# Kernel tuning notes

Hardware: AMD Instinct MI355X
Metric: run time of the kernel (lower is better)

Reference implementation:

```python
import jax, jax.numpy as jnp
import numpy as np
from jax import lax

B, L, D = 1, 2048, 768
D_IN, N, DT_RANK, K = 1536, 16, 48, 4
EPS = 1e-5


def setup_inputs() -> dict:
    key = jax.random.key(0)
    ks = jax.random.split(key, 10)
    s = 0.02
    x = jax.random.normal(ks[0], (B, L, D), dtype=jnp.float32)
    norm_w = jnp.ones((D,), dtype=jnp.float32)
    W_in = jax.random.normal(ks[1], (D, 2 * D_IN), dtype=jnp.float32) * s
    conv_w = jax.random.normal(ks[2], (K, 1, D_IN), dtype=jnp.float32) * s  # (W, I/groups, O)
    conv_b = jnp.zeros((D_IN,), dtype=jnp.float32)
    W_x = jax.random.normal(ks[3], (D_IN, DT_RANK + 2 * N), dtype=jnp.float32) * s
    W_dt = jax.random.normal(ks[4], (DT_RANK, D_IN), dtype=jnp.float32) * s
    b_dt = jnp.zeros((D_IN,), dtype=jnp.float32)
    A_log = jnp.broadcast_to(jnp.log(jnp.arange(1, N + 1, dtype=jnp.float32)), (D_IN, N))
    Dp = jnp.ones((D_IN,), dtype=jnp.float32)
    W_out = jax.random.normal(ks[5], (D_IN, D), dtype=jnp.float32) * s
    return {"x": x, "norm_w": norm_w, "W_in": W_in, "conv_w": conv_w, "conv_b": conv_b,
            "W_x": W_x, "W_dt": W_dt, "b_dt": b_dt, "A_log": A_log, "Dp": Dp, "W_out": W_out}


def _rmsnorm(x, w):
    return x * jax.lax.rsqrt(jnp.mean(x * x, axis=-1, keepdims=True) + EPS) * w


def _selective_scan(deltaA, deltaB_u, C):
    # deltaA, deltaB_u: (b, l, d_in, n); C: (b, l, n)
    def combine(s1, s2):
        f1, x1 = s1
        f2, x2 = s2
        return (f2 * f1, f2 * x1 + x2)
    _, xs = lax.associative_scan(combine, (deltaA, deltaB_u), axis=1)
    return jnp.einsum('bldn,bln->bld', xs, C)


def _mamba_block(x, W_in, conv_w, conv_b, W_x, W_dt, b_dt, A_log, Dp, W_out):
    b, l, d = x.shape
    xr = x @ W_in                                 # (b, l, 2*d_in)
    xs, res = jnp.split(xr, [D_IN], axis=-1)
    # depthwise causal-ish conv, padding = K-1 both sides, then trim to l
    xs = lax.conv_general_dilated(
        xs, conv_w, window_strides=(1,), padding=[(K - 1, K - 1)],
        dimension_numbers=('NWC', 'WIO', 'NWC'), feature_group_count=D_IN)
    xs = (xs + conv_b)[:, :l, :]
    u = jax.nn.silu(xs)
    # SSM
    A = -jnp.exp(A_log)                           # (d_in, n)
    x_dbl = u @ W_x                               # (b, l, dt_rank + 2n)
    delta, Bm, Cm = jnp.split(x_dbl, [DT_RANK, DT_RANK + N], axis=-1)
    delta = jax.nn.softplus(delta @ W_dt + b_dt)  # (b, l, d_in)
    deltaA = jnp.exp(jnp.einsum('bld,dn->bldn', delta, A))
    deltaB_u = jnp.einsum('bld,bln,bld->bldn', delta, Bm, u)
    y = _selective_scan(deltaA, deltaB_u, Cm) + u * Dp
    y = y * jax.nn.silu(res)
    return y @ W_out


def reference(x, norm_w, W_in, conv_w, conv_b, W_x, W_dt, b_dt, A_log, Dp, W_out):
    return _mamba_block(_rmsnorm(x, norm_w), W_in, conv_w, conv_b,
                        W_x, W_dt, b_dt, A_log, Dp, W_out) + x
```

## Files before the change

kernel.cpp:

```cpp
#include <hip/hip_runtime.h>
#include <hip/hip_bf16.h>

typedef unsigned short u16;
typedef __bf16 bfx8 __attribute__((ext_vector_type(8)));
typedef float fx4 __attribute__((ext_vector_type(4)));
typedef unsigned short ushort8 __attribute__((ext_vector_type(8)));

#define DEV __device__ __forceinline__

static constexpr int Lq = 2048, Dq = 768, DIN = 1536, NST = 16;
static constexpr int NCH = 128, LC = 16;

DEV u16 f2bf(float x) {
    union { float f; unsigned u; } v; v.f = x;
    unsigned r = v.u + 0x7fff + ((v.u >> 16) & 1);
    return (u16)(r >> 16);
}
DEV float bf2f(u16 v) {
    union { unsigned u; float f; } w; w.u = ((unsigned)v) << 16; return w.f;
}
DEV void gll16(const u16* g, u16* l) {
    __builtin_amdgcn_global_load_lds(
        (const __attribute__((address_space(1))) unsigned int*)g,
        (__attribute__((address_space(3))) unsigned int*)l, 16, 0, 0);
}

struct TD { const float* src; u16* dst; int R, C, Rp, Cp, nbx, blk0; };

__global__ __launch_bounds__(256) void prep(TD t0, TD t1, TD t2, TD t3,
                                            const float* __restrict__ x,
                                            const float* __restrict__ nw,
                                            u16* __restrict__ xn) {
    __shared__ float tile[32][33];
    __shared__ float wsum[4];
    int b = blockIdx.x;
    if (b < 3744) {
        TD td = t0;
        if (b >= t3.blk0) td = t3; else if (b >= t2.blk0) td = t2; else if (b >= t1.blk0) td = t1;
        int local = b - td.blk0;
        int c0 = (local % td.nbx) * 32, r0 = (local / td.nbx) * 32;
        int tx = threadIdx.x & 31, ty = threadIdx.x >> 5;
        #pragma unroll
        for (int i = ty; i < 32; i += 8) {
            int r = r0 + i, c = c0 + tx;
            tile[i][tx] = (r < td.R && c < td.C) ? td.src[(size_t)r * td.C + c] : 0.f;
        }
        __syncthreads();
        #pragma unroll
        for (int i = ty; i < 32; i += 8) {
            int c = c0 + i, r = r0 + tx;
            if (c < td.Cp && r < td.Rp) td.dst[(size_t)c * td.Rp + r] = f2bf(tile[tx][i]);
        }
    } else {
        int t = b - 3744;
        const float* row = x + (size_t)t * Dq;
        float ss = 0.f;
        for (int i = threadIdx.x; i < Dq; i += 256) { float a = row[i]; ss += a * a; }
        #pragma unroll
        for (int o = 32; o > 0; o >>= 1) ss += __shfl_xor(ss, o, 64);
        if ((threadIdx.x & 63) == 0) wsum[threadIdx.x >> 6] = ss;
        __syncthreads();
        ss = wsum[0] + wsum[1] + wsum[2] + wsum[3];
        float scale = rsqrtf(ss * (1.f / Dq) + 1e-5f);
        for (int i = threadIdx.x; i < Dq; i += 256)
            xn[(size_t)t * Dq + i] = f2bf(row[i] * scale * nw[i]);
    }
}

template<int BM, int BN, int EPI>
__global__ __launch_bounds__(256) void gemm_nt(const u16* __restrict__ A, const u16* __restrict__ BT,
                                               float* __restrict__ C, u16* __restrict__ Cb,
                                               const float* __restrict__ R,
                                               const float* __restrict__ bias,
                                               int M, int N, int K) {
    constexpr int BK = 64;
    constexpr int WM = BM / 2, WN = BN / 2, MI = WM / 16, NI = WN / 16;
    __shared__ u16 As[BM * BK];
    __shared__ u16 Bs[BN * BK];
    const int tid = threadIdx.x, lane = tid & 63, wid = tid >> 6;
    const int wr = wid >> 1, wc = wid & 1;
    const int bm0 = blockIdx.y * BM, bn0 = blockIdx.x * BN;
    const int li = lane & 15, g = lane >> 4;

    fx4 acc[MI][NI];
    #pragma unroll
    for (int mi = 0; mi < MI; mi++)
        #pragma unroll
        for (int ni = 0; ni < NI; ni++)
            #pragma unroll
            for (int q = 0; q < 4; q++) acc[mi][ni][q] = 0.f;

    for (int kt = 0; kt < K; kt += BK) {
        #pragma unroll
        for (int i = 0; i < (BM * 8) / 256; i++) {
            int cb = i * 256 + wid * 64;
            int c = cb + lane;
            int row = c >> 3, c16 = (c & 7) ^ (row & 7);
            gll16(A + (size_t)(bm0 + row) * K + kt + c16 * 8, &As[cb * 8]);
        }
        #pragma unroll
        for (int i = 0; i < (BN * 8) / 256; i++) {
            int cb = i * 256 + wid * 64;
            int c = cb + lane;
            int row = c >> 3, c16 = (c & 7) ^ (row & 7);
            gll16(BT + (size_t)(bn0 + row) * K + kt + c16 * 8, &Bs[cb * 8]);
        }
        __syncthreads();
        bfx8 af[MI][2], bfr[NI][2];
        #pragma unroll
        for (int mi = 0; mi < MI; mi++) {
            int row = wr * WM + mi * 16 + li;
            #pragma unroll
            for (int ks = 0; ks < 2; ks++)
                af[mi][ks] = *(const bfx8*)&As[row * BK + (((ks * 4 + g) ^ (row & 7)) * 8)];
        }
        #pragma unroll
        for (int ni = 0; ni < NI; ni++) {
            int row = wc * WN + ni * 16 + li;
            #pragma unroll
            for (int ks = 0; ks < 2; ks++)
                bfr[ni][ks] = *(const bfx8*)&Bs[row * BK + (((ks * 4 + g) ^ (row & 7)) * 8)];
        }
        #pragma unroll
        for (int ks = 0; ks < 2; ks++)
            #pragma unroll
            for (int mi = 0; mi < MI; mi++)
                #pragma unroll
                for (int ni = 0; ni < NI; ni++)
                    acc[mi][ni] = __builtin_amdgcn_mfma_f32_16x16x32_bf16(
                        af[mi][ks], bfr[ni][ks], acc[mi][ni], 0, 0, 0);
        __syncthreads();
    }

    #pragma unroll
    for (int mi = 0; mi < MI; mi++)
        #pragma unroll
        for (int ni = 0; ni < NI; ni++)
            #pragma unroll
            for (int q = 0; q < 4; q++) {
                int row = bm0 + wr * WM + mi * 16 + g * 4 + q;
                int col = bn0 + wc * WN + ni * 16 + li;
                size_t idx = (size_t)row * N + col;
                float v = acc[mi][ni][q];
                if constexpr (EPI == 0) {
                    if (R) v += R[idx];
                    C[idx] = v;
                } else if constexpr (EPI == 3) {
                    Cb[idx] = f2bf(v);
                } else if constexpr (EPI == 4) {
                    v += bias[col];
                    Cb[idx] = f2bf((v > 20.f) ? v : log1pf(__expf(v)));
                } else if constexpr (EPI == 5) {
                    C[idx] = v;
                    if (col < 64) Cb[(size_t)row * 64 + col] = f2bf(v);
                }
            }
}

__global__ __launch_bounds__(256) void conv_silu(const u16* __restrict__ xrb,
                                                 const float* __restrict__ cw,
                                                 const float* __restrict__ cb,
                                                 u16* __restrict__ ubf) {
    int i = blockIdx.x * 256 + threadIdx.x;
    int t = i / (DIN / 8), d8 = (i - t * (DIN / 8)) * 8;
    float acc[8];
    #pragma unroll
    for (int j = 0; j < 8; j++) acc[j] = cb[d8 + j];
    #pragma unroll
    for (int k = 0; k < 4; k++) {
        int tt = t - 3 + k;
        if (tt < 0) continue;
        ushort8 xv = *(const ushort8*)(xrb + (size_t)tt * (2 * DIN) + d8);
        #pragma unroll
        for (int j = 0; j < 8; j++) acc[j] = fmaf(bf2f(xv[j]), cw[k * DIN + d8 + j], acc[j]);
    }
    ushort8 o;
    #pragma unroll
    for (int j = 0; j < 8; j++) {
        float s = acc[j] / (1.f + __expf(-acc[j]));
        o[j] = f2bf(s);
    }
    *(ushort8*)(ubf + (size_t)i * 8) = o;
}

__global__ __launch_bounds__(256) void scan_p1(const u16* __restrict__ deltab, const u16* __restrict__ ubf,
                                               const float* __restrict__ xdbl, const float* __restrict__ A_log,
                                               float* __restrict__ chA, float* __restrict__ chX) {
    const int c = blockIdx.x;
    const int d = blockIdx.y * 256 + threadIdx.x;
    float An[NST];
    #pragma unroll
    for (int i = 0; i < 4; i++) {
        float4 a = *(const float4*)(A_log + (size_t)d * NST + i * 4);
        An[i * 4 + 0] = -__expf(a.x); An[i * 4 + 1] = -__expf(a.y);
        An[i * 4 + 2] = -__expf(a.z); An[i * 4 + 3] = -__expf(a.w);
    }
    float s[NST];
    #pragma unroll
    for (int n = 0; n < NST; n++) s[n] = 0.f;
    float sdl = 0.f;
    const int t0 = c * LC;
    #pragma unroll
    for (int tt = 0; tt < LC; tt++) {
        int t = t0 + tt;
        float dl = bf2f(deltab[(size_t)t * DIN + d]);
        float uu = bf2f(ubf[(size_t)t * DIN + d]);
        float dlu = dl * uu;
        #pragma unroll
        for (int i = 0; i < 4; i++) {
            float4 b = *(const float4*)(xdbl + (size_t)t * 128 + 48 + i * 4);
            float dA0 = __expf(dl * An[i*4+0]); s[i*4+0] = fmaf(dA0, s[i*4+0], dlu * b.x);
            float dA1 = __expf(dl * An[i*4+1]); s[i*4+1] = fmaf(dA1, s[i*4+1], dlu * b.y);
            float dA2 = __expf(dl * An[i*4+2]); s[i*4+2] = fmaf(dA2, s[i*4+2], dlu * b.z);
            float dA3 = __expf(dl * An[i*4+3]); s[i*4+3] = fmaf(dA3, s[i*4+3], dlu * b.w);
        }
        sdl += dl;
    }
    #pragma unroll
    for (int n = 0; n < NST; n++) {
        size_t idx = (size_t)n * (NCH * DIN) + (size_t)c * DIN + d;
        chX[idx] = s[n];
        chA[idx] = __expf(An[n] * sdl);
    }
}

__global__ __launch_bounds__(256) void scan_p2(float* __restrict__ chA, const float* __restrict__ chX) {
    int fid = blockIdx.x;
    int n = fid / 6, dd = (fid % 6) * 256 + threadIdx.x;
    size_t base = (size_t)n * (NCH * DIN) + dd;
    float s2 = 0.f;
    for (int cc = 0; cc < NCH; cc++) {
        size_t idx = base + (size_t)cc * DIN;
        float a = chA[idx], xv = chX[idx];
        chA[idx] = s2;
        s2 = fmaf(a, s2, xv);
    }
}

__global__ __launch_bounds__(256) void scan_p3(const u16* __restrict__ deltab, const u16* __restrict__ ubf,
                                               const float* __restrict__ xdbl, const float* __restrict__ A_log,
                                               const float* __restrict__ init, const float* __restrict__ Dp,
                                               const u16* __restrict__ xrb, u16* __restrict__ ybf) {
    const int c = blockIdx.x;
    const int d = blockIdx.y * 256 + threadIdx.x;
    float An[NST];
    #pragma unroll
    for (int i = 0; i < 4; i++) {
        float4 a = *(const float4*)(A_log + (size_t)d * NST + i * 4);
        An[i * 4 + 0] = -__expf(a.x); An[i * 4 + 1] = -__expf(a.y);
        An[i * 4 + 2] = -__expf(a.z); An[i * 4 + 3] = -__expf(a.w);
    }
    float s[NST];
    #pragma unroll
    for (int n = 0; n < NST; n++)
        s[n] = init[(size_t)n * (NCH * DIN) + (size_t)c * DIN + d];
    float Dpd = Dp[d];
    const int t0 = c * LC;
    #pragma unroll
    for (int tt = 0; tt < LC; tt++) {
        int t = t0 + tt;
        float dl = bf2f(deltab[(size_t)t * DIN + d]);
        float uu = bf2f(ubf[(size_t)t * DIN + d]);
        float dlu = dl * uu;
        float p = 0.f;
        #pragma unroll
        for (int i = 0; i < 4; i++) {
            float4 b  = *(const float4*)(xdbl + (size_t)t * 128 + 48 + i * 4);
            float4 cc = *(const float4*)(xdbl + (size_t)t * 128 + 64 + i * 4);
            float dA0 = __expf(dl * An[i*4+0]); s[i*4+0] = fmaf(dA0, s[i*4+0], dlu * b.x); p = fmaf(s[i*4+0], cc.x, p);
            float dA1 = __expf(dl * An[i*4+1]); s[i*4+1] = fmaf(dA1, s[i*4+1], dlu * b.y); p = fmaf(s[i*4+1], cc.y, p);
            float dA2 = __expf(dl * An[i*4+2]); s[i*4+2] = fmaf(dA2, s[i*4+2], dlu * b.z); p = fmaf(s[i*4+2], cc.z, p);
            float dA3 = __expf(dl * An[i*4+3]); s[i*4+3] = fmaf(dA3, s[i*4+3], dlu * b.w); p = fmaf(s[i*4+3], cc.w, p);
        }
        float res = bf2f(xrb[(size_t)t * (2 * DIN) + DIN + d]);
        float y = fmaf(uu, Dpd, p) * (res / (1.f + __expf(-res)));
        ybf[(size_t)t * DIN + d] = f2bf(y);
    }
}

extern "C" void kernel_launch(void* const* d_in, const int* in_sizes, int n_in,
                              void* d_out, int out_size, void* d_ws, size_t ws_size,
                              hipStream_t stream) {
    const float* x      = (const float*)d_in[0];
    const float* norm_w = (const float*)d_in[1];
    const float* W_in   = (const float*)d_in[2];
    const float* conv_w = (const float*)d_in[3];
    const float* conv_b = (const float*)d_in[4];
    const float* W_x    = (const float*)d_in[5];
    const float* W_dt   = (const float*)d_in[6];
    const float* b_dt   = (const float*)d_in[7];
    const float* A_log  = (const float*)d_in[8];
    const float* Dp     = (const float*)d_in[9];
    const float* W_out  = (const float*)d_in[10];
    float* out = (float*)d_out;

    char* wp = (char*)d_ws;
    auto alloc = [&](size_t bytes) { char* p = wp; wp += (bytes + 255) & ~(size_t)255; return p; };
    u16*      WinT   = (u16*)alloc((size_t)3072 * 768 * 2);
    u16*      WoutT  = (u16*)alloc((size_t)768 * 1536 * 2);
    u16*      WxT    = (u16*)alloc((size_t)128 * 1536 * 2);
    u16*      WdtT   = (u16*)alloc((size_t)1536 * 64 * 2);
    u16*      xn     = (u16*)alloc((size_t)Lq * Dq * 2);
    u16*      xrb    = (u16*)alloc((size_t)Lq * 3072 * 2);
    u16*      ubf    = (u16*)alloc((size_t)Lq * DIN * 2);
    float*    xdbl   = (float*)alloc((size_t)Lq * 128 * 4);
    u16*      draw   = (u16*)alloc((size_t)Lq * 64 * 2);
    u16*      deltab = (u16*)alloc((size_t)Lq * DIN * 2);
    float*    chA    = (float*)alloc((size_t)NCH * DIN * NST * 4);
    float*    chX    = (float*)alloc((size_t)NCH * DIN * NST * 4);
    u16*      ybf    = (u16*)alloc((size_t)Lq * DIN * 2);
    (void)ws_size; (void)in_sizes; (void)n_in; (void)out_size;

    TD t0{W_in,  WinT,  768, 3072,  768, 3072, 96,    0};
    TD t1{W_out, WoutT, 1536, 768, 1536,  768, 24, 2304};
    TD t2{W_x,   WxT,  1536,   80, 1536,  128,  4, 3456};
    TD t3{W_dt,  WdtT,   48, 1536,   64, 1536, 48, 3648};
    prep<<<3744 + Lq, 256, 0, stream>>>(t0, t1, t2, t3, x, norm_w, xn);

    gemm_nt<128, 128, 3><<<dim3(3072 / 128, Lq / 128), 256, 0, stream>>>(
        xn, WinT, nullptr, xrb, nullptr, nullptr, Lq, 3072, 768);

    conv_silu<<<(Lq * DIN / 8) / 256, 256, 0, stream>>>(xrb, conv_w, conv_b, ubf);

    gemm_nt<64, 64, 5><<<dim3(128 / 64, Lq / 64), 256, 0, stream>>>(
        ubf, WxT, xdbl, draw, nullptr, nullptr, Lq, 128, DIN);

    gemm_nt<128, 128, 4><<<dim3(1536 / 128, Lq / 128), 256, 0, stream>>>(
        draw, WdtT, nullptr, deltab, nullptr, b_dt, Lq, DIN, 64);

    scan_p1<<<dim3(NCH, DIN / 256), 256, 0, stream>>>(deltab, ubf, xdbl, A_log, chA, chX);
    scan_p2<<<96, 256, 0, stream>>>(chA, chX);
    scan_p3<<<dim3(NCH, DIN / 256), 256, 0, stream>>>(deltab, ubf, xdbl, A_log, chA, Dp, xrb, ybf);

    gemm_nt<128, 64, 0><<<dim3(Dq / 64, Lq / 128), 256, 0, stream>>>(
        ybf, WoutT, out, nullptr, x, nullptr, Lq, Dq, DIN);
}
```

Baseline: 230.9 us.

## Split-K the x_proj GEMM with atomics and read fp32 xdbl in dt GEMM

The thin x_proj GEMM (N=128, K=1536) is now split four ways along K. Partial sums are atomically added into an xdbl buffer that the prep kernel zeroes first. This is meant to fill far more CUs than the previous 64 blocks. The dt-projection GEMM now loads fp32 xdbl directly and converts it to bf16 while staging into LDS, which removes the separate draw buffer and its writes. The scan chunk count is also halved with longer chunks, and the timestep loops are no longer unrolled. This trades some scan parallelism for less inter-chunk work and adds atomic traffic and non-deterministic summation order.

Result: no change. 227.0 us (-1.7%).

```diff
diff --git a/kernel.cpp b/kernel.cpp
--- a/kernel.cpp
+++ b/kernel.cpp
@@ -9,7 +9,7 @@
 #define DEV __device__ __forceinline__
 
 static constexpr int Lq = 2048, Dq = 768, DIN = 1536, NST = 16;
-static constexpr int NCH = 128, LC = 16;
+static constexpr int NCH = 64, LC = 32;
 
 DEV u16 f2bf(float x) {
     union { float f; unsigned u; } v; v.f = x;
@@ -30,7 +30,8 @@
 __global__ __launch_bounds__(256) void prep(TD t0, TD t1, TD t2, TD t3,
                                             const float* __restrict__ x,
                                             const float* __restrict__ nw,
-                                            u16* __restrict__ xn) {
+                                            u16* __restrict__ xn,
+                                            float* __restrict__ xdbl) {
     __shared__ float tile[32][33];
     __shared__ float wsum[4];
     int b = blockIdx.x;
@@ -53,6 +54,7 @@
         }
     } else {
         int t = b - 3744;
+        if (threadIdx.x < 128) xdbl[(size_t)t * 128 + threadIdx.x] = 0.f;
         const float* row = x + (size_t)t * Dq;
         float ss = 0.f;
         for (int i = threadIdx.x; i < Dq; i += 256) { float a = row[i]; ss += a * a; }
@@ -67,12 +69,14 @@
     }
 }
 
-template<int BM, int BN, int EPI>
-__global__ __launch_bounds__(256) void gemm_nt(const u16* __restrict__ A, const u16* __restrict__ BT,
+template<int BM, int BN, int EPI, bool AF32 = false>
+__global__ __launch_bounds__(256) void gemm_nt(const u16* __restrict__ A,
+                                               const float* __restrict__ Af,
+                                               const u16* __restrict__ BT,
                                                float* __restrict__ C, u16* __restrict__ Cb,
                                                const float* __restrict__ R,
                                                const float* __restrict__ bias,
-                                               int M, int N, int K) {
+                                               int M, int N, int K, int kLen) {
     constexpr int BK = 64;
     constexpr int WM = BM / 2, WN = BN / 2, MI = WM / 16, NI = WN / 16;
     __shared__ u16 As[BM * BK];
@@ -80,6 +84,7 @@
     const int tid = threadIdx.x, lane = tid & 63, wid = tid >> 6;
     const int wr = wid >> 1, wc = wid & 1;
     const int bm0 = blockIdx.y * BM, bn0 = blockIdx.x * BN;
+    const int k0 = blockIdx.z * kLen;
     const int li = lane & 15, g = lane >> 4;
 
     fx4 acc[MI][NI];
@@ -90,20 +95,35 @@
             #pragma unroll
             for (int q = 0; q < 4; q++) acc[mi][ni][q] = 0.f;
 
-    for (int kt = 0; kt < K; kt += BK) {
-        #pragma unroll
-        for (int i = 0; i < (BM * 8) / 256; i++) {
-            int cb = i * 256 + wid * 64;
-            int c = cb + lane;
-            int row = c >> 3, c16 = (c & 7) ^ (row & 7);
-            gll16(A + (size_t)(bm0 + row) * K + kt + c16 * 8, &As[cb * 8]);
+    for (int kt = k0; kt < k0 + kLen; kt += BK) {
+        if constexpr (AF32) {
+            #pragma unroll
+            for (int i = 0; i < (BM * 8) / 256; i++) {
+                int c = i * 256 + tid;
+                int row = c >> 3, g16 = (c & 7) ^ (row & 7);
+                const float* src = Af + (size_t)(bm0 + row) * 128 + kt + g16 * 8;
+                float4 a0 = *(const float4*)src;
+                float4 a1 = *(const float4*)(src + 4);
+                ushort8 o;
+                o[0] = f2bf(a0.x); o[1] = f2bf(a0.y); o[2] = f2bf(a0.z); o[3] = f2bf(a0.w);
+                o[4] = f2bf(a1.x); o[5] = f2bf(a1.y); o[6] = f2bf(a1.z); o[7] = f2bf(a1.w);
+                *(ushort8*)(&As[c * 8]) = o;
+            }
+        } else {
+            #pragma unroll
+            for (int i = 0; i < (BM * 8) / 256; i++) {
+                int cb = i * 256 + wid * 64;
+                int c = cb + lane;
+                int row = c >> 3, g16 = (c & 7) ^ (row & 7);
+                gll16(A + (size_t)(bm0 + row) * K + kt + g16 * 8, &As[cb * 8]);
+            }
         }
         #pragma unroll
         for (int i = 0; i < (BN * 8) / 256; i++) {
             int cb = i * 256 + wid * 64;
             int c = cb + lane;
-            int row = c >> 3, c16 = (c & 7) ^ (row & 7);
-            gll16(BT + (size_t)(bn0 + row) * K + kt + c16 * 8, &Bs[cb * 8]);
+            int row = c >> 3, g16 = (c & 7) ^ (row & 7);
+            gll16(BT + (size_t)(bn0 + row) * K + kt + g16 * 8, &Bs[cb * 8]);
         }
         __syncthreads();
         bfx8 af[MI][2], bfr[NI][2];
@@ -145,14 +165,13 @@
                 if constexpr (EPI == 0) {
                     if (R) v += R[idx];
                     C[idx] = v;
+                } else if constexpr (EPI == 2) {
+                    atomicAdd(&C[idx], v);
                 } else if constexpr (EPI == 3) {
                     Cb[idx] = f2bf(v);
                 } else if constexpr (EPI == 4) {
                     v += bias[col];
                     Cb[idx] = f2bf((v > 20.f) ? v : log1pf(__expf(v)));
-                } else if constexpr (EPI == 5) {
-                    C[idx] = v;
-                    if (col < 64) Cb[(size_t)row * 64 + col] = f2bf(v);
                 }
             }
 }
@@ -200,7 +219,6 @@
     for (int n = 0; n < NST; n++) s[n] = 0.f;
     float sdl = 0.f;
     const int t0 = c * LC;
-    #pragma unroll
     for (int tt = 0; tt < LC; tt++) {
         int t = t0 + tt;
         float dl = bf2f(deltab[(size_t)t * DIN + d]);
@@ -256,7 +274,6 @@
         s[n] = init[(size_t)n * (NCH * DIN) + (size_t)c * DIN + d];
     float Dpd = Dp[d];
     const int t0 = c * LC;
-    #pragma unroll
     for (int tt = 0; tt < LC; tt++) {
         int t = t0 + tt;
         float dl = bf2f(deltab[(size_t)t * DIN + d]);
@@ -304,7 +321,6 @@
     u16*      xrb    = (u16*)alloc((size_t)Lq * 3072 * 2);
     u16*      ubf    = (u16*)alloc((size_t)Lq * DIN * 2);
     float*    xdbl   = (float*)alloc((size_t)Lq * 128 * 4);
-    u16*      draw   = (u16*)alloc((size_t)Lq * 64 * 2);
     u16*      deltab = (u16*)alloc((size_t)Lq * DIN * 2);
     float*    chA    = (float*)alloc((size_t)NCH * DIN * NST * 4);
     float*    chX    = (float*)alloc((size_t)NCH * DIN * NST * 4);
@@ -315,23 +331,23 @@
     TD t1{W_out, WoutT, 1536, 768, 1536,  768, 24, 2304};
     TD t2{W_x,   WxT,  1536,   80, 1536,  128,  4, 3456};
     TD t3{W_dt,  WdtT,   48, 1536,   64, 1536, 48, 3648};
-    prep<<<3744 + Lq, 256, 0, stream>>>(t0, t1, t2, t3, x, norm_w, xn);
+    prep<<<3744 + Lq, 256, 0, stream>>>(t0, t1, t2, t3, x, norm_w, xn, xdbl);
 
     gemm_nt<128, 128, 3><<<dim3(3072 / 128, Lq / 128), 256, 0, stream>>>(
-        xn, WinT, nullptr, xrb, nullptr, nullptr, Lq, 3072, 768);
+        xn, nullptr, WinT, nullptr, xrb, nullptr, nullptr, Lq, 3072, 768, 768);
 
     conv_silu<<<(Lq * DIN / 8) / 256, 256, 0, stream>>>(xrb, conv_w, conv_b, ubf);
 
-    gemm_nt<64, 64, 5><<<dim3(128 / 64, Lq / 64), 256, 0, stream>>>(
-        ubf, WxT, xdbl, draw, nullptr, nullptr, Lq, 128, DIN);
-
-    gemm_nt<128, 128, 4><<<dim3(1536 / 128, Lq / 128), 256, 0, stream>>>(
-        draw, WdtT, nullptr, deltab, nullptr, b_dt, Lq, DIN, 64);
+    gemm_nt<64, 64, 2><<<dim3(128 / 64, Lq / 64, 4), 256, 0, stream>>>(
+        ubf, nullptr, WxT, xdbl, nullptr, nullptr, nullptr, Lq, 128, DIN, 384);
+
+    gemm_nt<128, 128, 4, true><<<dim3(1536 / 128, Lq / 128), 256, 0, stream>>>(
+        nullptr, xdbl, WdtT, nullptr, deltab, nullptr, b_dt, Lq, DIN, 64, 64);
 
     scan_p1<<<dim3(NCH, DIN / 256), 256, 0, stream>>>(deltab, ubf, xdbl, A_log, chA, chX);
     scan_p2<<<96, 256, 0, stream>>>(chA, chX);
     scan_p3<<<dim3(NCH, DIN / 256), 256, 0, stream>>>(deltab, ubf, xdbl, A_log, chA, Dp, xrb, ybf);
 
     gemm_nt<128, 64, 0><<<dim3(Dq / 64, Lq / 128), 256, 0, stream>>>(
-        ybf, WoutT, out, nullptr, x, nullptr, Lq, Dq, DIN);
-}
+        ybf, nullptr, WoutT, out, nullptr, x, nullptr, Lq, Dq, DIN, DIN);
+}
```
